# Kernel optimization log

Hardware: AMD Instinct MI355X
Metric: run time of the kernel (lower is better)

The kernel has to match this reference:

```python
import jax, jax.numpy as jnp
import numpy as np

B, S, D, H = 4, 2048, 1024, 16
DK = D // H


def setup_inputs() -> dict:
    key = jax.random.key(0)
    ks = jax.random.split(key, 5)
    scale = 1.0 / np.sqrt(D)
    return {
        "embeddings": jax.random.normal(ks[0], (B, S, D), dtype=jnp.float32),
        "W_q": jax.random.normal(ks[1], (D, D), dtype=jnp.float32) * scale,
        "W_k": jax.random.normal(ks[2], (D, D), dtype=jnp.float32) * scale,
        "W_v": jax.random.normal(ks[3], (D, D), dtype=jnp.float32) * scale,
        "W_o": jax.random.normal(ks[4], (D, D), dtype=jnp.float32) * scale,
    }


def reference(embeddings, W_q, W_k, W_v, W_o):
    # torch Linear: y = x @ W.T  (weights stored [out, in])
    def proj(x, W):
        # [B,S,D] -> [B,H,S,DK]
        y = jnp.einsum("bsd,ed->bse", x, W)
        return y.reshape(B, S, H, DK).transpose(0, 2, 1, 3)

    Q = proj(embeddings, W_q)
    K = proj(embeddings, W_k)
    V = proj(embeddings, W_v)

    scores = jnp.einsum("bhqd,bhkd->bhqk", Q, K) / jnp.sqrt(jnp.float32(DK))
    p_attn = jax.nn.softmax(scores, axis=-1)  # dropout p=0.0 -> identity
    x = jnp.einsum("bhqk,bhkd->bhqd", p_attn, V)
    x = x.transpose(0, 2, 1, 3).reshape(B, S, D)
    return jnp.einsum("bsd,ed->bse", x, W_o)
```

## Files before the change

kernel.cpp:

```cpp
#include <hip/hip_runtime.h>
#include <hip/hip_bf16.h>

#define BB 4
#define SS 2048
#define DD 1024
#define HH 16
#define MM (BB * SS)

typedef __attribute__((ext_vector_type(8))) short bf16x8;
typedef __attribute__((ext_vector_type(4))) float f32x4;

__device__ __forceinline__ unsigned short f2bf(float f) {
  union { float f; unsigned u; } v; v.f = f;
  unsigned r = v.u + 0x7fffu + ((v.u >> 16) & 1u);
  return (unsigned short)(r >> 16);
}

__device__ __forceinline__ void gl2lds16(const void* g, void* l) {
  __builtin_amdgcn_global_load_lds(
      (const __attribute__((address_space(1))) unsigned int*)g,
      (__attribute__((address_space(3))) unsigned int*)l, 16, 0, 0);
}

__global__ __launch_bounds__(256)
void convall(const float* __restrict__ X, const float* __restrict__ a,
             const float* __restrict__ b, const float* __restrict__ c,
             const float* __restrict__ d, unsigned short* __restrict__ wall,
             unsigned short* __restrict__ xb) {
  int y = blockIdx.y;
  const float* s; unsigned short* o; float scl = 1.0f;
  if (y < 4) {
    const float* srcs[4] = {a, b, c, d};
    s = srcs[y]; o = wall + (size_t)y * 1048576;
    if (y == 0) scl = 0.180336880f;
  } else {
    s = X + (size_t)(y - 4) * 1048576; o = xb + (size_t)(y - 4) * 1048576;
  }
  int i = (blockIdx.x * 256 + threadIdx.x) * 4;
  float4 v = *(const float4*)(s + i);
  ushort4 h4;
  h4.x = f2bf(v.x * scl); h4.y = f2bf(v.y * scl);
  h4.z = f2bf(v.z * scl); h4.w = f2bf(v.w * scl);
  *(ushort4*)(o + i) = h4;
}

template<int OMODE>
__global__ __launch_bounds__(256)
void gemm_k(const unsigned short* __restrict__ A16, const unsigned short* __restrict__ Bp,
            void* __restrict__ C0p, void* __restrict__ C1p, void* __restrict__ C2p) {
  __shared__ unsigned short As[2 * 4096];
  __shared__ unsigned short Bs[2 * 4096];
  const int m0 = blockIdx.x * 128, n0g = blockIdx.y * 128;
  const int tid = threadIdx.x, lane = tid & 63, wave = tid >> 6;
  const int wm = (wave & 1) * 64, wn = (wave >> 1) * 64;
  const int row_in = lane & 15, quad = lane >> 4;

  f32x4 acc[4][4] = {};

  const int r = wave * 32 + (lane >> 2);
  const unsigned short* gB = Bp + (size_t)(n0g + r) * DD + (lane & 3) * 8;
  const unsigned short* gA = A16 + (size_t)(m0 + r) * DD + (lane & 3) * 8;

  gl2lds16(gB, Bs + (wave * 32) * 32);
  gl2lds16(gB + (size_t)16 * DD, Bs + (wave * 32 + 16) * 32);
  gl2lds16(gA, As + (wave * 32) * 32);
  gl2lds16(gA + (size_t)16 * DD, As + (wave * 32 + 16) * 32);

  int cur = 0;
  for (int kb = 0; kb < DD; kb += 32) {
    __syncthreads();
    if (kb + 32 < DD) {
      const int nx = (cur ^ 1) * 4096;
      gl2lds16(gB + kb + 32, Bs + nx + (wave * 32) * 32);
      gl2lds16(gB + kb + 32 + (size_t)16 * DD, Bs + nx + (wave * 32 + 16) * 32);
      gl2lds16(gA + kb + 32, As + nx + (wave * 32) * 32);
      gl2lds16(gA + kb + 32 + (size_t)16 * DD, As + nx + (wave * 32 + 16) * 32);
    }
    const int cb = cur * 4096;
    bf16x8 af[4], bfr[4];
#pragma unroll
    for (int i = 0; i < 4; ++i)
      af[i] = *(const bf16x8*)(As + cb + (wm + i * 16 + row_in) * 32 + quad * 8);
#pragma unroll
    for (int j = 0; j < 4; ++j)
      bfr[j] = *(const bf16x8*)(Bs + cb + (wn + j * 16 + row_in) * 32 + quad * 8);
    __builtin_amdgcn_s_setprio(1);
#pragma unroll
    for (int i = 0; i < 4; ++i)
#pragma unroll
      for (int j = 0; j < 4; ++j)
        acc[i][j] = __builtin_amdgcn_mfma_f32_16x16x32_bf16(af[i], bfr[j], acc[i][j], 0, 0, 0);
    __builtin_amdgcn_s_setprio(0);
    cur ^= 1;
  }
  __syncthreads();

  if (OMODE == 1) {
    float* Cout = (float*)C0p;
#pragma unroll
    for (int i = 0; i < 4; ++i)
#pragma unroll
      for (int j = 0; j < 4; ++j)
#pragma unroll
        for (int r2 = 0; r2 < 4; ++r2)
          Cout[(size_t)(m0 + wm + i * 16 + quad * 4 + r2) * DD + n0g + wn + j * 16 + row_in] =
              acc[i][j][r2];
  } else {
    const int seg = n0g >> 10;
    if (seg < 2) {
      unsigned short* Cout = (unsigned short*)(seg == 0 ? C0p : C1p);
      const int n0 = n0g & 1023;
#pragma unroll
      for (int i = 0; i < 4; ++i)
#pragma unroll
        for (int j = 0; j < 4; ++j)
#pragma unroll
          for (int r2 = 0; r2 < 4; ++r2)
            Cout[(size_t)(m0 + wm + i * 16 + quad * 4 + r2) * DD + n0 + wn + j * 16 + row_in] =
                f2bf(acc[i][j][r2]);
    } else {
      unsigned short* Vt = (unsigned short*)C2p;
      unsigned short* Ts = As;
      const int b = m0 >> 11, m_in_b = m0 & 2047;
      const int nv = n0g - 2048;
#pragma unroll
      for (int cn = 0; cn < 4; ++cn) {
        if ((wave >> 1) == (cn >> 1)) {
#pragma unroll
          for (int i = 0; i < 4; ++i)
#pragma unroll
            for (int jj = 0; jj < 2; ++jj)
#pragma unroll
              for (int r2 = 0; r2 < 4; ++r2) {
                int j = (cn & 1) * 2 + jj;
                Ts[(jj * 16 + row_in) * 136 + wm + i * 16 + quad * 4 + r2] = f2bf(acc[i][j][r2]);
              }
        }
        __syncthreads();
#pragma unroll
        for (int it = 0; it < 2; ++it) {
          int cc = tid + it * 256;
          int rowL = cc >> 4, o8 = (cc & 15) * 8;
          int cbase = rowL * 136 + (o8 & 64) + ((o8 & 63) >> 2);
          ushort4 lo, hi;
          lo.x = Ts[cbase];      lo.y = Ts[cbase + 16];
          lo.z = Ts[cbase + 32]; lo.w = Ts[cbase + 48];
          hi.x = Ts[cbase + 1];  hi.y = Ts[cbase + 17];
          hi.z = Ts[cbase + 33]; hi.w = Ts[cbase + 49];
          int n = nv + cn * 32 + rowL;
          int h = n >> 6, dd = n & 63;
          unsigned short* dst = Vt + ((size_t)((b * 16 + h) * 64 + dd)) * SS + m_in_b + o8;
          *(ushort4*)dst = lo;
          *(ushort4*)(dst + 4) = hi;
        }
        __syncthreads();
      }
    }
  }
}

__global__ __launch_bounds__(256, 4)
void attn_kernel(const unsigned short* __restrict__ Q, const unsigned short* __restrict__ K,
                 const unsigned short* __restrict__ Vt_g, unsigned short* __restrict__ AO) {
  __shared__ unsigned short Ks[64 * 72];
  __shared__ unsigned short Vs[64 * 72];
  __shared__ unsigned short Ps[128 * 72];
  const int L = (blockIdx.y << 4) + blockIdx.x;
  const int jj = L >> 3;
  const int qt = jj & 15;
  const int bh = (L & 7) + ((jj >> 4) << 3);
  const int b = bh >> 4, h = bh & 15;
  const int tid = threadIdx.x, lane = tid & 63, w = tid >> 6;
  const int row_in = lane & 15, quad = lane >> 4;
  const size_t qbase = ((size_t)(b * SS + qt * 128)) * DD + h * 64;

  bf16x8 aq[2][2];
#pragma unroll
  for (int m = 0; m < 2; ++m) {
    const unsigned short* qp = Q + qbase + (size_t)(w * 32 + m * 16 + row_in) * DD;
    aq[m][0] = *(const bf16x8*)(qp + quad * 8);
    aq[m][1] = *(const bf16x8*)(qp + 32 + quad * 8);
  }
  f32x4 oacc[2][4] = {};
  float lrow[2][4] = {};
  const int permr = 2 * (row_in >> 2) + (row_in & 1) + 8 * ((row_in >> 1) & 1);
  const int pw_base = (w * 32) * 72;

  const int r0 = tid >> 3, o80 = (tid & 7) * 8;
  const int r1 = (tid + 256) >> 3, o81 = o80;
  const unsigned short* kp0 = K + ((size_t)(b * SS + r0)) * DD + h * 64 + o80;
  const unsigned short* kp1 = K + ((size_t)(b * SS + r1)) * DD + h * 64 + o81;
  const unsigned short* vp0 = Vt_g + ((size_t)(bh * 64 + r0)) * SS + o80;
  const unsigned short* vp1 = Vt_g + ((size_t)(bh * 64 + r1)) * SS + o81;

  uint4 kr0 = *(const uint4*)kp0;
  uint4 kr1 = *(const uint4*)kp1;
  uint4 vr0 = *(const uint4*)vp0;
  uint4 vr1 = *(const uint4*)vp1;

  for (int kt = 0; kt < SS / 64; ++kt) {
    __syncthreads();
    *(uint4*)(Ks + r0 * 72 + o80) = kr0;
    *(uint4*)(Ks + r1 * 72 + o81) = kr1;
    *(uint4*)(Vs + r0 * 72 + o80) = vr0;
    *(uint4*)(Vs + r1 * 72 + o81) = vr1;
    __syncthreads();
    if (kt + 1 < SS / 64) {
      const size_t ko = (size_t)(kt + 1) * 64 * DD;
      const size_t vo = (size_t)(kt + 1) * 64;
      kr0 = *(const uint4*)(kp0 + ko);
      kr1 = *(const uint4*)(kp1 + ko);
      vr0 = *(const uint4*)(vp0 + vo);
      vr1 = *(const uint4*)(vp1 + vo);
    }

    f32x4 sacc[2][4] = {};
    __builtin_amdgcn_s_setprio(1);
#pragma unroll
    for (int n = 0; n < 4; ++n) {
      bf16x8 bk0 = *(const bf16x8*)(Ks + (n * 16 + row_in) * 72 + quad * 8);
      bf16x8 bk1 = *(const bf16x8*)(Ks + (n * 16 + row_in) * 72 + 32 + quad * 8);
#pragma unroll
      for (int m = 0; m < 2; ++m) {
        sacc[m][n] = __builtin_amdgcn_mfma_f32_16x16x32_bf16(aq[m][0], bk0, sacc[m][n], 0, 0, 0);
        sacc[m][n] = __builtin_amdgcn_mfma_f32_16x16x32_bf16(aq[m][1], bk1, sacc[m][n], 0, 0, 0);
      }
    }
    __builtin_amdgcn_s_setprio(0);

#pragma unroll
    for (int m = 0; m < 2; ++m)
#pragma unroll
      for (int r = 0; r < 4; ++r) {
        int prow = pw_base + (m * 16 + 2 * quad + (r & 1) + 8 * ((r >> 1) & 1)) * 72;
        union { float f; unsigned u; } p0, p1, p2, p3;
        p0.f = __builtin_amdgcn_exp2f(sacc[m][0][r]);
        p1.f = __builtin_amdgcn_exp2f(sacc[m][1][r]);
        p2.f = __builtin_amdgcn_exp2f(sacc[m][2][r]);
        p3.f = __builtin_amdgcn_exp2f(sacc[m][3][r]);
        lrow[m][r] += (p0.f + p1.f) + (p2.f + p3.f);
        unsigned w01 = __builtin_amdgcn_perm(p1.u + 0x8000u, p0.u + 0x8000u, 0x07060302);
        unsigned w23 = __builtin_amdgcn_perm(p3.u + 0x8000u, p2.u + 0x8000u, 0x07060302);
        *(uint2*)(Ps + prow + row_in * 4) = make_uint2(w01, w23);
      }

    __builtin_amdgcn_s_setprio(1);
#pragma unroll
    for (int c = 0; c < 2; ++c) {
      bf16x8 ap0 = *(const bf16x8*)(Ps + pw_base + (permr) * 72 + c * 32 + quad * 8);
      bf16x8 ap1 = *(const bf16x8*)(Ps + pw_base + (16 + permr) * 72 + c * 32 + quad * 8);
#pragma unroll
      for (int t = 0; t < 4; ++t) {
        bf16x8 bv = *(const bf16x8*)(Vs + (t * 16 + row_in) * 72 + c * 32 + quad * 8);
        oacc[0][t] = __builtin_amdgcn_mfma_f32_16x16x32_bf16(ap0, bv, oacc[0][t], 0, 0, 0);
        oacc[1][t] = __builtin_amdgcn_mfma_f32_16x16x32_bf16(ap1, bv, oacc[1][t], 0, 0, 0);
      }
    }
    __builtin_amdgcn_s_setprio(0);
  }

#pragma unroll
  for (int m = 0; m < 2; ++m)
#pragma unroll
    for (int r = 0; r < 4; ++r) {
#pragma unroll
      for (int s = 1; s < 16; s <<= 1) lrow[m][r] += __shfl_xor(lrow[m][r], s, 64);
      float inv = 1.0f / lrow[m][r];
#pragma unroll
      for (int t = 0; t < 4; ++t)
        AO[qbase + (size_t)(w * 32 + m * 16 + quad * 4 + r) * DD + t * 16 + row_in] =
            f2bf(oacc[m][t][r] * inv);
    }
}

extern "C" void kernel_launch(void* const* d_in, const int* in_sizes, int n_in,
                              void* d_out, int out_size, void* d_ws, size_t ws_size,
                              hipStream_t stream) {
  const float* X  = (const float*)d_in[0];
  const float* Wq = (const float*)d_in[1];
  const float* Wk = (const float*)d_in[2];
  const float* Wv = (const float*)d_in[3];
  const float* Wo = (const float*)d_in[4];

  unsigned short* ws   = (unsigned short*)d_ws;
  unsigned short* Qb   = ws;
  unsigned short* Kb   = Qb + (size_t)MM * DD;
  unsigned short* Vtb  = Kb + (size_t)MM * DD;
  unsigned short* Wall = Vtb + (size_t)MM * DD;
  unsigned short* Xb   = (unsigned short*)d_out;
  float* out = (float*)d_out;

  convall<<<dim3(1024, 12), 256, 0, stream>>>(X, Wq, Wk, Wv, Wo, Wall, Xb);

  gemm_k<3><<<dim3(MM / 128, 24), 256, 0, stream>>>(Xb, Wall, Qb, Kb, Vtb);

  attn_kernel<<<dim3(SS / 128, BB * HH), 256, 0, stream>>>(Qb, Kb, Vtb, Qb);

  gemm_k<1><<<dim3(MM / 128, 8), 256, 0, stream>>>(Qb, Wall + (size_t)3 * 1048576,
                                                   out, nullptr, nullptr);
}
```

Measured before the change: 263.2 us.

## Triple-buffer GEMM LDS tiles with explicit vmcnt waits for deeper prefetch

Expands the GEMM's shared-memory staging from double to triple buffering, so global-to-LDS loads run two K-tiles ahead. The per-iteration __syncthreads becomes an explicit s_waitcnt vmcnt(4) plus s_barrier, so only the oldest tile's loads are awaited. This aims to hide more global memory latency behind the MFMA work. It costs 50% more LDS per block, which may lower occupancy, and it depends on the hand-written vmcnt count matching the outstanding loads.

```diff
diff --git a/kernel.cpp b/kernel.cpp
--- a/kernel.cpp
+++ b/kernel.cpp
@@ -48,8 +48,8 @@
 __global__ __launch_bounds__(256)
 void gemm_k(const unsigned short* __restrict__ A16, const unsigned short* __restrict__ Bp,
             void* __restrict__ C0p, void* __restrict__ C1p, void* __restrict__ C2p) {
-  __shared__ unsigned short As[2 * 4096];
-  __shared__ unsigned short Bs[2 * 4096];
+  __shared__ unsigned short As[3 * 4096];
+  __shared__ unsigned short Bs[3 * 4096];
   const int m0 = blockIdx.x * 128, n0g = blockIdx.y * 128;
   const int tid = threadIdx.x, lane = tid & 63, wave = tid >> 6;
   const int wm = (wave & 1) * 64, wn = (wave >> 1) * 64;
@@ -60,30 +60,38 @@
   const int r = wave * 32 + (lane >> 2);
   const unsigned short* gB = Bp + (size_t)(n0g + r) * DD + (lane & 3) * 8;
   const unsigned short* gA = A16 + (size_t)(m0 + r) * DD + (lane & 3) * 8;
-
-  gl2lds16(gB, Bs + (wave * 32) * 32);
-  gl2lds16(gB + (size_t)16 * DD, Bs + (wave * 32 + 16) * 32);
-  gl2lds16(gA, As + (wave * 32) * 32);
-  gl2lds16(gA + (size_t)16 * DD, As + (wave * 32 + 16) * 32);
-
-  int cur = 0;
-  for (int kb = 0; kb < DD; kb += 32) {
-    __syncthreads();
-    if (kb + 32 < DD) {
-      const int nx = (cur ^ 1) * 4096;
-      gl2lds16(gB + kb + 32, Bs + nx + (wave * 32) * 32);
-      gl2lds16(gB + kb + 32 + (size_t)16 * DD, Bs + nx + (wave * 32 + 16) * 32);
-      gl2lds16(gA + kb + 32, As + nx + (wave * 32) * 32);
-      gl2lds16(gA + kb + 32 + (size_t)16 * DD, As + nx + (wave * 32 + 16) * 32);
-    }
-    const int cb = cur * 4096;
+  const int wrow0 = (wave * 32) * 32, wrow1 = (wave * 32 + 16) * 32;
+
+#define STAGE_G(t, bo)                                         \
+  do {                                                         \
+    const int kb_ = (t) * 32;                                  \
+    gl2lds16(gB + kb_, Bs + (bo) + wrow0);                     \
+    gl2lds16(gB + kb_ + (size_t)16 * DD, Bs + (bo) + wrow1);   \
+    gl2lds16(gA + kb_, As + (bo) + wrow0);                     \
+    gl2lds16(gA + kb_ + (size_t)16 * DD, As + (bo) + wrow1);   \
+  } while (0)
+
+  STAGE_G(0, 0);
+  STAGE_G(1, 4096);
+
+  int bo_rd = 0;
+  int bo_st = 8192;
+  const int NT = DD / 32;
+  for (int t = 0; t < NT; ++t) {
+    if (t < NT - 1) {
+      asm volatile("s_waitcnt vmcnt(4)" ::: "memory");
+    } else {
+      asm volatile("s_waitcnt vmcnt(0)" ::: "memory");
+    }
+    __builtin_amdgcn_s_barrier();
+    if (t + 2 < NT) STAGE_G(t + 2, bo_st);
     bf16x8 af[4], bfr[4];
 #pragma unroll
     for (int i = 0; i < 4; ++i)
-      af[i] = *(const bf16x8*)(As + cb + (wm + i * 16 + row_in) * 32 + quad * 8);
+      af[i] = *(const bf16x8*)(As + bo_rd + (wm + i * 16 + row_in) * 32 + quad * 8);
 #pragma unroll
     for (int j = 0; j < 4; ++j)
-      bfr[j] = *(const bf16x8*)(Bs + cb + (wn + j * 16 + row_in) * 32 + quad * 8);
+      bfr[j] = *(const bf16x8*)(Bs + bo_rd + (wn + j * 16 + row_in) * 32 + quad * 8);
     __builtin_amdgcn_s_setprio(1);
 #pragma unroll
     for (int i = 0; i < 4; ++i)
@@ -91,8 +99,10 @@
       for (int j = 0; j < 4; ++j)
         acc[i][j] = __builtin_amdgcn_mfma_f32_16x16x32_bf16(af[i], bfr[j], acc[i][j], 0, 0, 0);
     __builtin_amdgcn_s_setprio(0);
-    cur ^= 1;
-  }
+    bo_rd = (bo_rd == 8192) ? 0 : bo_rd + 4096;
+    bo_st = (bo_st == 8192) ? 0 : bo_st + 4096;
+  }
+#undef STAGE_G
   __syncthreads();
 
   if (OMODE == 1) {
```

Result: slower. 283.8 us (+7.8%).

## Use 256x256 tiled QKV GEMM with swizzled LDS and separate V transpose

Applied to the files above, without the earlier changes.

Replaces the 128x128 QKV projection GEMM with a 512-thread 256x256 tile kernel. It uses 128KB of dynamic LDS, XOR-swizzled layout, a hand-scheduled double-buffered pipeline with explicit vmcnt waits, and a grouped block order for L2 locality. The fused V-transpose epilogue is removed. V is now written row-major into the output buffer and transposed by a separate small kernel. This trades an extra launch and a round trip of V through memory for higher arithmetic intensity and fewer syncs in the main GEMM.

```diff
diff --git a/kernel.cpp b/kernel.cpp
--- a/kernel.cpp
+++ b/kernel.cpp
@@ -44,10 +44,166 @@
   *(ushort4*)(o + i) = h4;
 }
 
-template<int OMODE>
+__global__ __launch_bounds__(512, 2)
+void gemm256(const unsigned short* __restrict__ A16, const unsigned short* __restrict__ Bp,
+             unsigned short* __restrict__ Qo, unsigned short* __restrict__ Ko,
+             unsigned short* __restrict__ Vo) {
+  extern __shared__ unsigned short L[];
+  const int Lid = blockIdx.x;
+  const int wg = (Lid & 7) * 48 + (Lid >> 3);
+  const int mx = wg & 31, ny = wg >> 5;
+  const int m0 = mx * 256, n0g = ny * 256;
+
+  const int tid = threadIdx.x, lane = tid & 63, wv = tid >> 6;
+  const int wave_m = wv >> 2, wave_n = wv & 3;
+  const int row_in = lane & 15, quad = lane >> 4;
+
+  const int srow = lane >> 3;
+  const int sc = ((lane & 7) ^ (lane >> 3)) * 8;
+  const unsigned short* gA0 = A16 + (size_t)(m0 + srow) * DD + sc;
+  const unsigned short* gB0 = Bp + (size_t)(n0g + srow) * DD + sc;
+
+  const int aoff = (wave_m * 128 + row_in) * 64;
+  const int boff = (wave_n * 64 + row_in) * 64;
+  const int swz0 = ((quad) ^ (row_in & 7)) * 8;
+  const int swz1 = ((4 + quad) ^ (row_in & 7)) * 8;
+
+  f32x4 acc[8][4] = {};
+
+#define SA(a, par, kbv)                                                         \
+  do {                                                                          \
+    const int ld_ = (par) * 16384 + (a) * 8192 + (wv * 16) * 64;                \
+    gl2lds16(gA0 + (size_t)((a) * 128 + wv * 16 + 0) * DD + (kbv), L + ld_);    \
+    gl2lds16(gA0 + (size_t)((a) * 128 + wv * 16 + 8) * DD + (kbv), L + ld_ + 512); \
+  } while (0)
+#define SBf(par, kbv)                                                           \
+  do {                                                                          \
+    const int ld_ = 32768 + (par) * 16384 + (wv * 32) * 64;                     \
+    gl2lds16(gB0 + (size_t)(wv * 32 + 0) * DD + (kbv), L + ld_);                \
+    gl2lds16(gB0 + (size_t)(wv * 32 + 8) * DD + (kbv), L + ld_ + 512);          \
+    gl2lds16(gB0 + (size_t)(wv * 32 + 16) * DD + (kbv), L + ld_ + 1024);        \
+    gl2lds16(gB0 + (size_t)(wv * 32 + 24) * DD + (kbv), L + ld_ + 1536);        \
+  } while (0)
+#define LDA(par, mh, swzv)                                                      \
+  do {                                                                          \
+    _Pragma("unroll") for (int f = 0; f < 4; ++f)                               \
+        af[f] = *(const bf16x8*)(L + (par) * 16384 + aoff + ((mh) * 64 + f * 16) * 64 + (swzv)); \
+  } while (0)
+#define LDB(par, swzv)                                                          \
+  do {                                                                          \
+    _Pragma("unroll") for (int nf = 0; nf < 4; ++nf)                            \
+        bk[nf] = *(const bf16x8*)(L + 32768 + (par) * 16384 + boff + nf * 1024 + (swzv)); \
+  } while (0)
+#define MFMA16(mh)                                                              \
+  do {                                                                          \
+    __builtin_amdgcn_s_setprio(1);                                              \
+    _Pragma("unroll") for (int f = 0; f < 4; ++f)                               \
+        _Pragma("unroll") for (int nf = 0; nf < 4; ++nf)                        \
+            acc[(mh) * 4 + f][nf] = __builtin_amdgcn_mfma_f32_16x16x32_bf16(    \
+                af[f], bk[nf], acc[(mh) * 4 + f][nf], 0, 0, 0);                 \
+    __builtin_amdgcn_s_setprio(0);                                              \
+  } while (0)
+#define PBAR()                                 \
+  do {                                         \
+    asm volatile("" ::: "memory");             \
+    __builtin_amdgcn_s_barrier();              \
+    asm volatile("" ::: "memory");             \
+  } while (0)
+#define PWAIT(n) asm volatile("s_waitcnt vmcnt(" #n ")" ::: "memory")
+
+  SA(0, 0, 0);
+  SBf(0, 0);
+  SA(1, 0, 0);
+  SA(0, 1, 64);
+
+  for (int i = 0; i < 8; ++i) {
+    const int kb1 = (2 * i + 1) * 64;
+    const int t2 = 2 * i + 2, t3 = 2 * i + 3;
+    const int kb2 = (t2 < 16 ? t2 : 15) * 64;
+    const int kb3 = (t3 < 16 ? t3 : 15) * 64;
+    bf16x8 af[4], bk[4];
+    PWAIT(4); PBAR();
+    LDB(0, swz0); LDA(0, 0, swz0);
+    SBf(1, kb1);
+    MFMA16(0);
+    PWAIT(6); PBAR();
+    LDA(0, 1, swz0);
+    SA(1, 1, kb1);
+    MFMA16(1);
+    PBAR();
+    LDB(0, swz1); LDA(0, 0, swz1);
+    MFMA16(0);
+    PBAR();
+    LDA(0, 1, swz1);
+    SA(0, 0, kb2);
+    MFMA16(1);
+    PWAIT(4); PBAR();
+    LDB(1, swz0); LDA(1, 0, swz0);
+    SBf(0, kb2);
+    MFMA16(0);
+    PWAIT(6); PBAR();
+    LDA(1, 1, swz0);
+    SA(1, 0, kb2);
+    MFMA16(1);
+    PBAR();
+    LDB(1, swz1); LDA(1, 0, swz1);
+    MFMA16(0);
+    PBAR();
+    LDA(1, 1, swz1);
+    SA(0, 1, kb3);
+    MFMA16(1);
+  }
+  asm volatile("s_waitcnt vmcnt(0)" ::: "memory");
+#undef SA
+#undef SBf
+#undef LDA
+#undef LDB
+#undef MFMA16
+#undef PBAR
+#undef PWAIT
+
+  const int seg = n0g >> 10;
+  unsigned short* Cout = (seg == 0) ? Qo : (seg == 1) ? Ko : Vo;
+  const int n0 = n0g & 1023;
+#pragma unroll
+  for (int mh = 0; mh < 2; ++mh)
+#pragma unroll
+    for (int f = 0; f < 4; ++f)
+#pragma unroll
+      for (int nf = 0; nf < 4; ++nf)
+#pragma unroll
+        for (int r2 = 0; r2 < 4; ++r2)
+          Cout[(size_t)(m0 + wave_m * 128 + mh * 64 + f * 16 + quad * 4 + r2) * DD +
+               n0 + wave_n * 64 + nf * 16 + row_in] = f2bf(acc[mh * 4 + f][nf][r2]);
+}
+
 __global__ __launch_bounds__(256)
-void gemm_k(const unsigned short* __restrict__ A16, const unsigned short* __restrict__ Bp,
-            void* __restrict__ C0p, void* __restrict__ C1p, void* __restrict__ C2p) {
+void vtrans(const unsigned short* __restrict__ V, unsigned short* __restrict__ Vt) {
+  __shared__ unsigned short T[64][66];
+  const int kt = blockIdx.x, bh = blockIdx.y, b = bh >> 4, h = bh & 15;
+  const int t = threadIdx.x;
+  const unsigned short* src = V + ((size_t)(b * SS + kt * 64)) * DD + h * 64;
+#pragma unroll
+  for (int it = 0; it < 2; ++it) {
+    int key = (t >> 3) + it * 32, c8 = (t & 7) * 8;
+    *(uint4*)&T[key][c8] = *(const uint4*)(src + (size_t)key * DD + c8);
+  }
+  __syncthreads();
+#pragma unroll
+  for (int it = 0; it < 4; ++it) {
+    int d = (t >> 4) + it * 16, pc = t & 15;
+    ushort4 v;
+    v.x = T[pc + 0][d];
+    v.y = T[pc + 16][d];
+    v.z = T[pc + 32][d];
+    v.w = T[pc + 48][d];
+    *(ushort4*)(Vt + ((size_t)(bh * 64 + d)) * SS + kt * 64 + pc * 4) = v;
+  }
+}
+
+__global__ __launch_bounds__(256)
+void gemm_o(const unsigned short* __restrict__ A16, const unsigned short* __restrict__ Bp,
+            float* __restrict__ Cout) {
   __shared__ unsigned short As[2 * 4096];
   __shared__ unsigned short Bs[2 * 4096];
   const int m0 = blockIdx.x * 128, n0g = blockIdx.y * 128;
@@ -95,68 +251,14 @@
   }
   __syncthreads();
 
-  if (OMODE == 1) {
-    float* Cout = (float*)C0p;
-#pragma unroll
-    for (int i = 0; i < 4; ++i)
-#pragma unroll
-      for (int j = 0; j < 4; ++j)
-#pragma unroll
-        for (int r2 = 0; r2 < 4; ++r2)
-          Cout[(size_t)(m0 + wm + i * 16 + quad * 4 + r2) * DD + n0g + wn + j * 16 + row_in] =
-              acc[i][j][r2];
-  } else {
-    const int seg = n0g >> 10;
-    if (seg < 2) {
-      unsigned short* Cout = (unsigned short*)(seg == 0 ? C0p : C1p);
-      const int n0 = n0g & 1023;
-#pragma unroll
-      for (int i = 0; i < 4; ++i)
-#pragma unroll
-        for (int j = 0; j < 4; ++j)
-#pragma unroll
-          for (int r2 = 0; r2 < 4; ++r2)
-            Cout[(size_t)(m0 + wm + i * 16 + quad * 4 + r2) * DD + n0 + wn + j * 16 + row_in] =
-                f2bf(acc[i][j][r2]);
-    } else {
-      unsigned short* Vt = (unsigned short*)C2p;
-      unsigned short* Ts = As;
-      const int b = m0 >> 11, m_in_b = m0 & 2047;
-      const int nv = n0g - 2048;
-#pragma unroll
-      for (int cn = 0; cn < 4; ++cn) {
-        if ((wave >> 1) == (cn >> 1)) {
-#pragma unroll
-          for (int i = 0; i < 4; ++i)
-#pragma unroll
-            for (int jj = 0; jj < 2; ++jj)
-#pragma unroll
-              for (int r2 = 0; r2 < 4; ++r2) {
-                int j = (cn & 1) * 2 + jj;
-                Ts[(jj * 16 + row_in) * 136 + wm + i * 16 + quad * 4 + r2] = f2bf(acc[i][j][r2]);
-              }
-        }
-        __syncthreads();
-#pragma unroll
-        for (int it = 0; it < 2; ++it) {
-          int cc = tid + it * 256;
-          int rowL = cc >> 4, o8 = (cc & 15) * 8;
-          int cbase = rowL * 136 + (o8 & 64) + ((o8 & 63) >> 2);
-          ushort4 lo, hi;
-          lo.x = Ts[cbase];      lo.y = Ts[cbase + 16];
-          lo.z = Ts[cbase + 32]; lo.w = Ts[cbase + 48];
-          hi.x = Ts[cbase + 1];  hi.y = Ts[cbase + 17];
-          hi.z = Ts[cbase + 33]; hi.w = Ts[cbase + 49];
-          int n = nv + cn * 32 + rowL;
-          int h = n >> 6, dd = n & 63;
-          unsigned short* dst = Vt + ((size_t)((b * 16 + h) * 64 + dd)) * SS + m_in_b + o8;
-          *(ushort4*)dst = lo;
-          *(ushort4*)(dst + 4) = hi;
-        }
-        __syncthreads();
-      }
-    }
-  }
+#pragma unroll
+  for (int i = 0; i < 4; ++i)
+#pragma unroll
+    for (int j = 0; j < 4; ++j)
+#pragma unroll
+      for (int r2 = 0; r2 < 4; ++r2)
+        Cout[(size_t)(m0 + wm + i * 16 + quad * 4 + r2) * DD + n0g + wn + j * 16 + row_in] =
+            acc[i][j][r2];
 }
 
 __global__ __launch_bounds__(256, 4)
@@ -288,14 +390,23 @@
   unsigned short* Vtb  = Kb + (size_t)MM * DD;
   unsigned short* Wall = Vtb + (size_t)MM * DD;
   unsigned short* Xb   = (unsigned short*)d_out;
+  unsigned short* Vb   = (unsigned short*)d_out + (size_t)MM * DD;
   float* out = (float*)d_out;
 
+  static int inited = 0;
+  if (!inited) {
+    hipFuncSetAttribute((const void*)gemm256,
+                        hipFuncAttributeMaxDynamicSharedMemorySize, 131072);
+    inited = 1;
+  }
+
   convall<<<dim3(1024, 12), 256, 0, stream>>>(X, Wq, Wk, Wv, Wo, Wall, Xb);
 
-  gemm_k<3><<<dim3(MM / 128, 24), 256, 0, stream>>>(Xb, Wall, Qb, Kb, Vtb);
+  gemm256<<<dim3(384), 512, 131072, stream>>>(Xb, Wall, Qb, Kb, Vb);
+
+  vtrans<<<dim3(SS / 64, BB * HH), 256, 0, stream>>>(Vb, Vtb);
 
   attn_kernel<<<dim3(SS / 128, BB * HH), 256, 0, stream>>>(Qb, Kb, Vtb, Qb);
 
-  gemm_k<1><<<dim3(MM / 128, 8), 256, 0, stream>>>(Qb, Wall + (size_t)3 * 1048576,
-                                                   out, nullptr, nullptr);
-}
+  gemm_o<<<dim3(MM / 128, 8), 256, 0, stream>>>(Qb, Wall + (size_t)3 * 1048576, out);
+}
```

After: 265.5 us. Within noise of the previous version (+0.9%).
